# Optimization experiments

Measured on AMD Instinct MI355X. Metric: run time of the kernel, lower is better.

The kernel has to match this reference:

```python
import jax, jax.numpy as jnp
import numpy as np
from jax.ops import segment_sum, segment_max

N, F, H, HEADS, E, OUT = 50000, 256, 64, 4, 800000, 16


def setup_inputs() -> dict:
    key = jax.random.key(0)
    ks = jax.random.split(key, 16)
    s = 0.05
    return {
        "x": jax.random.normal(ks[0], (N, F), jnp.float32),
        "edge_index": jax.random.randint(ks[1], (2, E), 0, N, jnp.int64),
        # GCN layer params
        "W_gcn1": jax.random.normal(ks[2], (F, H), jnp.float32) * s,
        "b_gcn1": jnp.zeros((H,), jnp.float32),
        "W_gcn2": jax.random.normal(ks[3], (H, OUT), jnp.float32) * s,
        "b_gcn2": jnp.zeros((OUT,), jnp.float32),
        # GAT layer 1 (heads=HEADS, concat)
        "W_gat1": jax.random.normal(ks[4], (F, HEADS * H), jnp.float32) * s,
        "a_src1": jax.random.normal(ks[5], (HEADS, H), jnp.float32) * s,
        "a_dst1": jax.random.normal(ks[6], (HEADS, H), jnp.float32) * s,
        "b_gat1": jnp.zeros((HEADS * H,), jnp.float32),
        # GAT layer 2 (heads=1, concat=False)
        "W_gat2": jax.random.normal(ks[7], (HEADS * H, OUT), jnp.float32) * s,
        "a_src2": jax.random.normal(ks[8], (1, OUT), jnp.float32) * s,
        "a_dst2": jax.random.normal(ks[9], (1, OUT), jnp.float32) * s,
        "b_gat2": jnp.zeros((OUT,), jnp.float32),
    }


def _add_self_loops(edge_index, n):
    loop = jnp.arange(n, dtype=edge_index.dtype)
    src = jnp.concatenate([edge_index[0], loop])
    dst = jnp.concatenate([edge_index[1], loop])
    return src, dst


def _gcn(x, src, dst, norm, W, b, n):
    h = x @ W  # [N, out]
    out = segment_sum(h[src] * norm[:, None], dst, num_segments=n)
    return out + b


def _gat(x, src, dst, W, a_s, a_d, b, heads, concat, n):
    h = (x @ W).reshape(n, heads, -1)  # [N, heads, C]
    s_src = jnp.einsum("nhc,hc->nh", h, a_s)
    s_dst = jnp.einsum("nhc,hc->nh", h, a_d)
    e = jax.nn.leaky_relu(s_src[src] + s_dst[dst], 0.2)  # [Etot, heads]
    m = segment_max(e, dst, num_segments=n)               # per-dst softmax
    p = jnp.exp(e - m[dst])
    denom = segment_sum(p, dst, num_segments=n)
    alpha = p / denom[dst]
    out = segment_sum(h[src] * alpha[..., None], dst, num_segments=n)
    out = out.reshape(n, -1) if concat else out.mean(axis=1)
    return out + b


def reference(x, edge_index, W_gcn1, b_gcn1, W_gcn2, b_gcn2,
              W_gat1, a_src1, a_dst1, b_gat1,
              W_gat2, a_src2, a_dst2, b_gat2):
    n = x.shape[0]
    src, dst = _add_self_loops(edge_index, n)
    # symmetric GCN normalization on self-loop-augmented graph
    deg = segment_sum(jnp.ones_like(dst, x.dtype), dst, num_segments=n)
    dinv = jnp.where(deg > 0, jax.lax.rsqrt(deg), 0.0)
    norm = dinv[src] * dinv[dst]

    x_gcn = jax.nn.relu(_gcn(x, src, dst, norm, W_gcn1, b_gcn1, n))
    x_gcn = _gcn(x_gcn, src, dst, norm, W_gcn2, b_gcn2, n)

    x_gat = jax.nn.relu(_gat(x, src, dst, W_gat1, a_src1, a_dst1, b_gat1, HEADS, True, n))
    x_gat = _gat(x_gat, src, dst, W_gat2, a_src2, a_dst2, b_gat2, 1, False, n)

    return jnp.concatenate([x_gcn, x_gat], axis=1)
```

## Files before the change

kernel.cpp:

```cpp
#include <hip/hip_runtime.h>
#include <math.h>

#define NN     50000
#define FF     256
#define HH     64
#define NHEADS 4
#define EE     800000
#define OUTD   16

typedef __attribute__((ext_vector_type(8))) short short8;
typedef __attribute__((ext_vector_type(4))) float f32x4;

__device__ inline unsigned short f2bf(float f) {
    unsigned u = __builtin_bit_cast(unsigned, f);
    unsigned r = (u + 0x7fff + ((u >> 16) & 1)) >> 16;
    return (unsigned short)r;
}
__device__ inline float bf2f(unsigned short s) {
    unsigned u = ((unsigned)s) << 16;
    return __builtin_bit_cast(float, u);
}

__device__ inline void pack_one(const float* __restrict__ W,
                                unsigned short* __restrict__ bhi,
                                unsigned short* __restrict__ blo,
                                int t_, int NT, int NTOT, int TOFF, int SRC_NC) {
    int lane = t_ & 63;
    int tile = (t_ >> 6) % NT;
    int kb = (t_ >> 6) / NT;
    int q = lane >> 4, c = lane & 15;
    size_t off = ((size_t)(kb * NTOT + TOFF + tile) * 64 + lane) * 8;
#pragma unroll
    for (int j = 0; j < 8; j++) {
        float w = W[(size_t)(kb * 32 + q * 8 + j) * SRC_NC + tile * 16 + c];
        unsigned short h = f2bf(w);
        bhi[off + j] = h;
        if (blo) blo[off + j] = f2bf(w - bf2f(h));
    }
}

#define NTT 20
__global__ __launch_bounds__(256) void k_prep(const float* __restrict__ Wg1,
                                              const float* __restrict__ Wgat1,
                                              const float* __restrict__ Wg2,
                                              const float* __restrict__ Wgat2,
                                              unsigned short* __restrict__ bhiC,
                                              unsigned short* __restrict__ bhiG2,
                                              unsigned short* __restrict__ bloG2,
                                              unsigned short* __restrict__ bhiA2,
                                              unsigned short* __restrict__ bloA2,
                                              int* __restrict__ cnt) {
    int t = blockIdx.x * 256 + threadIdx.x;
    if (t < NN) cnt[t] = 0;
    if (t < 2048)        pack_one(Wg1,   bhiC,  nullptr, t,         4,  NTT, 0, 64);
    else if (t < 10240)  pack_one(Wgat1, bhiC,  nullptr, t - 2048,  16, NTT, 4, 256);
    else if (t < 10368)  pack_one(Wg2,   bhiG2, bloG2,   t - 10240, 1,  1,   0, 16);
    else if (t < 10880)  pack_one(Wgat2, bhiA2, bloA2,   t - 10368, 1,  1,   0, 16);
}

__global__ void k_count(const int* __restrict__ dst, int* __restrict__ cnt, int e) {
    int i = blockIdx.x * blockDim.x + threadIdx.x;
    if (i < e) atomicAdd(&cnt[dst[i]], 1);
}

__global__ __launch_bounds__(256) void k_scan_a(const int* __restrict__ cnt,
                                                int* __restrict__ partial, int n) {
    int i = blockIdx.x * 256 + threadIdx.x;
    int v = (i < n) ? cnt[i] : 0;
#pragma unroll
    for (int off = 32; off >= 1; off >>= 1) v += __shfl_xor(v, off, 64);
    __shared__ int ws[4];
    int wave = threadIdx.x >> 6;
    if ((threadIdx.x & 63) == 0) ws[wave] = v;
    __syncthreads();
    if (threadIdx.x == 0) partial[blockIdx.x] = ws[0] + ws[1] + ws[2] + ws[3];
}

__global__ __launch_bounds__(256) void k_scan_b(const int* __restrict__ partial,
                                                int* __restrict__ blockoff,
                                                int* __restrict__ total_out, int nb) {
    __shared__ int arr[256];
    int tid = threadIdx.x;
    arr[tid] = (tid < nb) ? partial[tid] : 0;
    __syncthreads();
#pragma unroll
    for (int off = 1; off < 256; off <<= 1) {
        int v = arr[tid];
        int add = (tid >= off) ? arr[tid - off] : 0;
        __syncthreads();
        arr[tid] = v + add;
        __syncthreads();
    }
    if (tid < nb) blockoff[tid] = arr[tid] - partial[tid];
    if (tid == 0) *total_out = arr[255];
}

__global__ __launch_bounds__(256) void k_scan_c(const int* __restrict__ cnt,
                                                const int* __restrict__ blockoff,
                                                int* __restrict__ row_start,
                                                int* __restrict__ cursor,
                                                float* __restrict__ dinv, int n) {
    __shared__ int arr[256];
    int tid = threadIdx.x;
    int i = blockIdx.x * 256 + tid;
    int c = (i < n) ? cnt[i] : 0;
    arr[tid] = c;
    __syncthreads();
#pragma unroll
    for (int off = 1; off < 256; off <<= 1) {
        int v = arr[tid];
        int add = (tid >= off) ? arr[tid - off] : 0;
        __syncthreads();
        arr[tid] = v + add;
        __syncthreads();
    }
    if (i < n) {
        int excl = arr[tid] - c + blockoff[blockIdx.x];
        row_start[i] = excl;
        cursor[i] = excl;
        dinv[i] = rsqrtf((float)(c + 1));
    }
}

__global__ void k_fill(const int* __restrict__ src, const int* __restrict__ dst,
                       int* __restrict__ cursor, int* __restrict__ col, int e) {
    int i = blockIdx.x * blockDim.x + threadIdx.x;
    if (i < e) {
        int d = dst[i];
        int pos = atomicAdd(&cursor[d], 1);
        col[pos] = src[i];
    }
}

__global__ __launch_bounds__(512, 4) void mfma_gemm_fused(const float* __restrict__ A,
                                                       const unsigned short* __restrict__ Bhi,
                                                       unsigned short* __restrict__ Ch1,
                                                       unsigned char* __restrict__ Chg,
                                                       float* __restrict__ scl,
                                                       const float* __restrict__ dinv,
                                                       const float* __restrict__ a_s,
                                                       const float* __restrict__ a_d,
                                                       float* __restrict__ ssrc,
                                                       float* __restrict__ sdst,
                                                       int M) {
    const int K = 256;
    int tid = threadIdx.x;
    int w = tid >> 6, lane = tid & 63, q = lane >> 4, c = lane & 15;
    int rg = w & 3;
    int half = w >> 2;
    const int T0 = half * 10;
    int row_base = blockIdx.x * 64 + rg * 16;
    int ar = min(row_base + c, M - 1);
    const float* ap = A + (size_t)ar * K + q * 8;

    __shared__ unsigned short ldsB[2][NTT * 512];

    auto stage = [&](int kb, int buf) {
        const char* srcb = (const char*)Bhi + (size_t)kb * (NTT * 1024);
#pragma unroll
        for (int cch = 0; cch < 3; cch++) {
            int ch = w + cch * 8;
            if (ch < NTT) {
                __builtin_amdgcn_global_load_lds(
                    (const unsigned int*)(srcb + ch * 1024 + lane * 16),
                    (unsigned int*)((char*)&ldsB[buf][0] + ch * 1024),
                    16, 0, 0);
            }
        }
    };

    f32x4 acc[10];
#pragma unroll
    for (int t = 0; t < 10; t++) acc[t] = (f32x4){0.f, 0.f, 0.f, 0.f};

    float av[8];
    *(float4*)(av)     = *(const float4*)(ap);
    *(float4*)(av + 4) = *(const float4*)(ap + 4);
    stage(0, 0);
    __syncthreads();

    int buf = 0;
#pragma unroll
    for (int kb = 0; kb < 8; kb++) {
        if (kb < 7) stage(kb + 1, buf ^ 1);
        short8 ahi, alo;
#pragma unroll
        for (int j = 0; j < 8; j++) {
            unsigned short h = f2bf(av[j]);
            ahi[j] = (short)h;
            alo[j] = (short)f2bf(av[j] - bf2f(h));
        }
        if (kb < 7) {
            *(float4*)(av)     = *(const float4*)(ap + (kb + 1) * 32);
            *(float4*)(av + 4) = *(const float4*)(ap + (kb + 1) * 32 + 4);
        }
        const char* bbase = (const char*)&ldsB[buf][0] + lane * 16;
#pragma unroll
        for (int lt = 0; lt < 10; lt++) {
            short8 b = *(const short8*)(bbase + (size_t)(T0 + lt) * 1024);
            acc[lt] = __builtin_amdgcn_mfma_f32_16x16x32_bf16(ahi, b, acc[lt], 0, 0, 0);
            acc[lt] = __builtin_amdgcn_mfma_f32_16x16x32_bf16(alo, b, acc[lt], 0, 0, 0);
        }
        __syncthreads();
        buf ^= 1;
    }

    __shared__ float s_ss[2][64][4];
    __shared__ float s_sd[2][64][4];
    __shared__ float s_mx[2][64];

#pragma unroll
    for (int i = 0; i < 4; i++) {
        int lr = rg * 16 + q * 4 + i;
        float ss[4] = {0.f, 0.f, 0.f, 0.f};
        float sd[4] = {0.f, 0.f, 0.f, 0.f};
        float m = 0.f;
#pragma unroll
        for (int lt = 0; lt < 10; lt++) {
            int gt = T0 + lt;
            if (gt >= 4) {
                int t = gt - 4;
                float v = acc[lt][i];
                ss[t >> 2] += v * a_s[t * 16 + c];
                sd[t >> 2] += v * a_d[t * 16 + c];
                m = fmaxf(m, fabsf(v));
            }
        }
#pragma unroll
        for (int h = 0; h < 4; h++) {
#pragma unroll
            for (int off = 1; off <= 8; off <<= 1) {
                ss[h] += __shfl_xor(ss[h], off, 16);
                sd[h] += __shfl_xor(sd[h], off, 16);
            }
        }
#pragma unroll
        for (int off = 1; off <= 8; off <<= 1) m = fmaxf(m, __shfl_xor(m, off, 16));
        if (c == i) {
#pragma unroll
            for (int h = 0; h < 4; h++) {
                s_ss[half][lr][h] = ss[h];
                s_sd[half][lr][h] = sd[h];
            }
            s_mx[half][lr] = m;
        }
    }
    __syncthreads();

#pragma unroll
    for (int i = 0; i < 4; i++) {
        int lr = rg * 16 + q * 4 + i;
        int r = row_base + q * 4 + i;
        float m = fmaxf(fmaxf(s_mx[0][lr], s_mx[1][lr]), 1e-20f);
        float inv = 127.0f / m;
        if (half == 0 && c == i && r < M) {
            *(float4*)(ssrc + (size_t)r * 4) =
                make_float4(s_ss[0][lr][0] + s_ss[1][lr][0], s_ss[0][lr][1] + s_ss[1][lr][1],
                            s_ss[0][lr][2] + s_ss[1][lr][2], s_ss[0][lr][3] + s_ss[1][lr][3]);
            *(float4*)(sdst + (size_t)r * 4) =
                make_float4(s_sd[0][lr][0] + s_sd[1][lr][0], s_sd[0][lr][1] + s_sd[1][lr][1],
                            s_sd[0][lr][2] + s_sd[1][lr][2], s_sd[0][lr][3] + s_sd[1][lr][3]);
            scl[r] = m * (1.0f / 127.0f);
        }
        if (r < M) {
            if (half == 0) {
                float sc = dinv[r];
#pragma unroll
                for (int lt = 0; lt < 4; lt++)
                    Ch1[(size_t)r * 64 + lt * 16 + c] = f2bf(acc[lt][i] * sc);
            }
#pragma unroll
            for (int lt = 0; lt < 10; lt++) {
                int gt = T0 + lt;
                if (gt >= 4) {
                    int t = gt - 4;
                    int qv = (int)rintf(acc[lt][i] * inv) + 128;
                    Chg[(size_t)r * 256 + t * 16 + c] = (unsigned char)qv;
                }
            }
        }
    }
}

template <int KB, bool SCALE, bool SC2, int OFS>
__device__ inline void n16_body(int bx, int tid,
                                const unsigned short* __restrict__ A,
                                const unsigned short* __restrict__ Bhi,
                                const unsigned short* __restrict__ Blo,
                                unsigned short* __restrict__ Cbf,
                                const float* __restrict__ rowscale,
                                const float* __restrict__ a_s2,
                                const float* __restrict__ a_d2,
                                float* __restrict__ s2s,
                                float* __restrict__ s2d, int M) {
    const int K = KB * 32;
    int w = tid >> 6, lane = tid & 63, q = lane >> 4, c = lane & 15;
    int row_base = bx * 64 + w * 16;
    int ar = min(row_base + c, M - 1);
    const unsigned short* ap = A + (size_t)ar * K + q * 8;
    f32x4 acc = (f32x4){0.f, 0.f, 0.f, 0.f};
#pragma unroll
    for (int kb = 0; kb < KB; kb++) {
        short8 av = *(const short8*)(ap + kb * 32);
        size_t bo = ((size_t)kb * 64 + lane) * 8;
        short8 bh = *(const short8*)(Bhi + bo);
        short8 bl = *(const short8*)(Blo + bo);
        acc = __builtin_amdgcn_mfma_f32_16x16x32_bf16(av, bh, acc, 0, 0, 0);
        acc = __builtin_amdgcn_mfma_f32_16x16x32_bf16(av, bl, acc, 0, 0, 0);
    }
    if (SC2) {
#pragma unroll
        for (int i = 0; i < 4; i++) {
            float ps = acc[i] * a_s2[c];
            float pd = acc[i] * a_d2[c];
#pragma unroll
            for (int off = 1; off <= 8; off <<= 1) {
                ps += __shfl_xor(ps, off, 16);
                pd += __shfl_xor(pd, off, 16);
            }
            int r = row_base + q * 4 + i;
            if (c == i && r < M) {
                s2s[r] = ps;
                s2d[r] = pd;
            }
        }
    }
#pragma unroll
    for (int i = 0; i < 4; i++) {
        int r = row_base + q * 4 + i;
        if (r < M) {
            float sc = SCALE ? rowscale[r] : 1.0f;
            Cbf[((size_t)r * 16 + c) * 2 + OFS] = f2bf(acc[i] * sc);
        }
    }
}

__global__ __launch_bounds__(256) void mfma_n16_both(const unsigned short* __restrict__ Ag,
                                                     const unsigned short* __restrict__ Ac,
                                                     const unsigned short* __restrict__ bhiA2,
                                                     const unsigned short* __restrict__ bloA2,
                                                     const unsigned short* __restrict__ bhiG2,
                                                     const unsigned short* __restrict__ bloG2,
                                                     unsigned short* __restrict__ pairb,
                                                     const float* __restrict__ dinv,
                                                     const float* __restrict__ a_s2,
                                                     const float* __restrict__ a_d2,
                                                     float* __restrict__ s2s,
                                                     float* __restrict__ s2d,
                                                     int M, int GB) {
    int bx = blockIdx.x;
    if (bx < GB)
        n16_body<8, false, true, 1>(bx, threadIdx.x, Ag, bhiA2, bloA2, pairb,
                                    nullptr, a_s2, a_d2, s2s, s2d, M);
    else
        n16_body<2, true, false, 0>(bx - GB, threadIdx.x, Ac, bhiG2, bloG2, pairb,
                                    dinv, nullptr, nullptr, nullptr, nullptr, M);
}

__global__ __launch_bounds__(256) void both_agg(const unsigned char* __restrict__ hg,
                                                const unsigned short* __restrict__ h1,
                                                const float* __restrict__ scl,
                                                const int* __restrict__ rs,
                                                const int* __restrict__ col,
                                                const float* __restrict__ ssrc,
                                                const float* __restrict__ sdst,
                                                const float* __restrict__ dinv,
                                                const float* __restrict__ bgat,
                                                const float* __restrict__ bgcn,
                                                unsigned short* __restrict__ outg,
                                                unsigned short* __restrict__ outc) {
    __shared__ int s_lds[4][64];
    __shared__ float p_lds[4][64 * 4];
    int tid = threadIdx.x;
    int w = tid >> 6, lane = tid & 63;
    int wid = blockIdx.x * 4 + w;
    int hh = lane >> 4;
    int cidx = (lane & 15) * 4;
    int* sl = s_lds[w];
    float* pl = p_lds[w];

    float di = dinv[wid];
    float4 sd4 = *(const float4*)(sdst + (size_t)wid * 4);
    float sdv[4] = {sd4.x, sd4.y, sd4.z, sd4.w};
    float4 sf4 = *(const float4*)(ssrc + (size_t)wid * 4);
    float sfv[4] = {sf4.x, sf4.y, sf4.z, sf4.w};
    float psf[4];
#pragma unroll
    for (int h = 0; h < 4; h++) {
        float e = sfv[h] + sdv[h];
        e = (e >= 0.f) ? e : 0.2f * e;
        psf[h] = __expf(e);
    }
    float pse = (hh & 2) ? ((hh & 1) ? psf[3] : psf[2]) : ((hh & 1) ? psf[1] : psf[0]);
    float pses = pse * scl[wid];
    const unsigned char* hbase = hg + lane * 4;
    unsigned hv0 = *(const unsigned*)(hbase + (size_t)wid * 256);
    float4 acc;
    acc.x = ((float)(hv0 & 0xffu) - 128.f) * pses;
    acc.y = ((float)((hv0 >> 8) & 0xffu) - 128.f) * pses;
    acc.z = ((float)((hv0 >> 16) & 0xffu) - 128.f) * pses;
    acc.w = ((float)(hv0 >> 24) - 128.f) * pses;
    float accb = 0.f;
    float4 accc = make_float4(0.f, 0.f, 0.f, 0.f);

    float lsum[4] = {0.f, 0.f, 0.f, 0.f};
    int beg = rs[wid], end = rs[wid + 1];
    for (int j0 = beg; j0 < end; j0 += 64) {
        int cnt = min(64, end - j0);
        if (lane < cnt) {
            int sreg = col[j0 + lane];
            float ssc = scl[sreg];
            float4 sv = *(const float4*)(ssrc + (size_t)sreg * 4);
            float svv[4] = {sv.x, sv.y, sv.z, sv.w};
            float pv[4];
#pragma unroll
            for (int h = 0; h < 4; h++) {
                float e = svv[h] + sdv[h];
                e = (e >= 0.f) ? e : 0.2f * e;
                pv[h] = __expf(e);
                lsum[h] += pv[h];
            }
            sl[lane] = sreg;
            *(float4*)&pl[lane * 4] =
                make_float4(pv[0] * ssc, pv[1] * ssc, pv[2] * ssc, pv[3] * ssc);
        }
        int e = 0;
        for (; e + 4 <= cnt; e += 4) {
            int s0 = sl[e], s1 = sl[e + 1], s2 = sl[e + 2], s3 = sl[e + 3];
            float p0 = pl[e * 4 + hh], p1 = pl[(e + 1) * 4 + hh];
            float p2 = pl[(e + 2) * 4 + hh], p3 = pl[(e + 3) * 4 + hh];
            unsigned v0 = *(const unsigned*)(hbase + (size_t)s0 * 256);
            unsigned v1 = *(const unsigned*)(hbase + (size_t)s1 * 256);
            unsigned v2 = *(const unsigned*)(hbase + (size_t)s2 * 256);
            unsigned v3 = *(const unsigned*)(hbase + (size_t)s3 * 256);
            acc.x += (float)(v0 & 0xffu) * p0;
            acc.y += (float)((v0 >> 8) & 0xffu) * p0;
            acc.z += (float)((v0 >> 16) & 0xffu) * p0;
            acc.w += (float)(v0 >> 24) * p0;
            acc.x += (float)(v1 & 0xffu) * p1;
            acc.y += (float)((v1 >> 8) & 0xffu) * p1;
            acc.z += (float)((v1 >> 16) & 0xffu) * p1;
            acc.w += (float)(v1 >> 24) * p1;
            acc.x += (float)(v2 & 0xffu) * p2;
            acc.y += (float)((v2 >> 8) & 0xffu) * p2;
            acc.z += (float)((v2 >> 16) & 0xffu) * p2;
            acc.w += (float)(v2 >> 24) * p2;
            acc.x += (float)(v3 & 0xffu) * p3;
            acc.y += (float)((v3 >> 8) & 0xffu) * p3;
            acc.z += (float)((v3 >> 16) & 0xffu) * p3;
            acc.w += (float)(v3 >> 24) * p3;
            accb += (p0 + p1) + (p2 + p3);
        }
        for (; e < cnt; e++) {
            int s = sl[e];
            float p = pl[e * 4 + hh];
            unsigned v = *(const unsigned*)(hbase + (size_t)s * 256);
            acc.x += (float)(v & 0xffu) * p;
            acc.y += (float)((v >> 8) & 0xffu) * p;
            acc.z += (float)((v >> 16) & 0xffu) * p;
            acc.w += (float)(v >> 24) * p;
            accb += p;
        }
        int e2 = hh;
        for (; e2 + 4 < cnt; e2 += 8) {
            int sa = sl[e2], sb = sl[e2 + 4];
            ushort4 va = *(const ushort4*)(h1 + (size_t)sa * HH + cidx);
            ushort4 vb = *(const ushort4*)(h1 + (size_t)sb * HH + cidx);
            accc.x += bf2f(va.x) + bf2f(vb.x);
            accc.y += bf2f(va.y) + bf2f(vb.y);
            accc.z += bf2f(va.z) + bf2f(vb.z);
            accc.w += bf2f(va.w) + bf2f(vb.w);
        }
        if (e2 < cnt) {
            int sa = sl[e2];
            ushort4 va = *(const ushort4*)(h1 + (size_t)sa * HH + cidx);
            accc.x += bf2f(va.x); accc.y += bf2f(va.y);
            accc.z += bf2f(va.z); accc.w += bf2f(va.w);
        }
    }
    float corr = 128.0f * accb;
    acc.x -= corr; acc.y -= corr; acc.z -= corr; acc.w -= corr;
#pragma unroll
    for (int h = 0; h < 4; h++) {
        float v = lsum[h];
        for (int off = 32; off >= 1; off >>= 1) v += __shfl_xor(v, off, 64);
        lsum[h] = v + psf[h];
    }
    float lt = (hh & 2) ? ((hh & 1) ? lsum[3] : lsum[2]) : ((hh & 1) ? lsum[1] : lsum[0]);
    float li = 1.0f / lt;
    float4 bv = *(const float4*)(bgat + lane * 4);
    ushort4 o;
    o.x = f2bf(fmaxf(acc.x * li + bv.x, 0.f));
    o.y = f2bf(fmaxf(acc.y * li + bv.y, 0.f));
    o.z = f2bf(fmaxf(acc.z * li + bv.z, 0.f));
    o.w = f2bf(fmaxf(acc.w * li + bv.w, 0.f));
    *(ushort4*)(outg + (size_t)wid * 256 + lane * 4) = o;
#pragma unroll
    for (int off = 16; off <= 32; off <<= 1) {
        accc.x += __shfl_xor(accc.x, off, 64);
        accc.y += __shfl_xor(accc.y, off, 64);
        accc.z += __shfl_xor(accc.z, off, 64);
        accc.w += __shfl_xor(accc.w, off, 64);
    }
    if (hh == 0) {
        ushort4 sv = *(const ushort4*)(h1 + (size_t)wid * HH + cidx);
        float4 bc = *(const float4*)(bgcn + cidx);
        ushort4 oc;
        oc.x = f2bf(fmaxf((accc.x + bf2f(sv.x)) * di + bc.x, 0.f));
        oc.y = f2bf(fmaxf((accc.y + bf2f(sv.y)) * di + bc.y, 0.f));
        oc.z = f2bf(fmaxf((accc.z + bf2f(sv.z)) * di + bc.z, 0.f));
        oc.w = f2bf(fmaxf((accc.w + bf2f(sv.w)) * di + bc.w, 0.f));
        *(ushort4*)(outc + (size_t)wid * HH + cidx) = oc;
    }
}

__global__ __launch_bounds__(256) void final_agg(const unsigned* __restrict__ hp,
                                                 const int* __restrict__ rs,
                                                 const int* __restrict__ col,
                                                 const float* __restrict__ dinv,
                                                 const float* __restrict__ s2s,
                                                 const float* __restrict__ s2d,
                                                 const float* __restrict__ bg2,
                                                 const float* __restrict__ bga2,
                                                 float* __restrict__ out) {
    int t = blockIdx.x * 256 + threadIdx.x;
    int node = t >> 4;
    int c = t & 15;
    float di = dinv[node];
    float sd = s2d[node];
    float es = s2s[node] + sd;
    es = (es >= 0.f) ? es : 0.2f * es;
    float psf = __expf(es);
    unsigned pvs = hp[(size_t)node * 16 + c];
    float accg = bf2f((unsigned short)pvs);
    float acca = bf2f((unsigned short)(pvs >> 16)) * psf;
    float lp = 0.f;
    int beg = rs[node], end = rs[node + 1];
    for (int j0 = beg; j0 < end; j0 += 16) {
        int cnt = min(16, end - j0);
        int sreg = 0;
        float pr = 0.f;
        if (c < cnt) {
            sreg = col[j0 + c];
            float e = s2s[sreg] + sd;
            e = (e >= 0.f) ? e : 0.2f * e;
            pr = __expf(e);
            lp += pr;
        }
        for (int e = 0; e < cnt; e += 4) {
            int si[4];
            float pi[4];
#pragma unroll
            for (int u = 0; u < 4; u++) {
                si[u] = __shfl(sreg, (e + u) & 15, 16);
                pi[u] = __shfl(pr, (e + u) & 15, 16);
            }
            unsigned hv[4];
#pragma unroll
            for (int u = 0; u < 4; u++) hv[u] = hp[(size_t)si[u] * 16 + c];
#pragma unroll
            for (int u = 0; u < 4; u++) {
                if (e + u < cnt) {
                    accg += bf2f((unsigned short)hv[u]);
                    acca += bf2f((unsigned short)(hv[u] >> 16)) * pi[u];
                }
            }
        }
    }
    for (int off = 8; off >= 1; off >>= 1) lp += __shfl_xor(lp, off, 16);
    float l = lp + psf;
    out[(size_t)node * 32 + c] = accg * di + bg2[c];
    out[(size_t)node * 32 + 16 + c] = acca / l + bga2[c];
}

extern "C" void kernel_launch(void* const* d_in, const int* in_sizes, int n_in,
                              void* d_out, int out_size, void* d_ws, size_t ws_size,
                              hipStream_t stream) {
    const float* x      = (const float*)d_in[0];
    const int*   ei     = (const int*)d_in[1];
    const float* Wg1    = (const float*)d_in[2];
    const float* bg1    = (const float*)d_in[3];
    const float* Wg2    = (const float*)d_in[4];
    const float* bg2    = (const float*)d_in[5];
    const float* Wgat1  = (const float*)d_in[6];
    const float* a_src1 = (const float*)d_in[7];
    const float* a_dst1 = (const float*)d_in[8];
    const float* bgat1  = (const float*)d_in[9];
    const float* Wgat2  = (const float*)d_in[10];
    const float* a_src2 = (const float*)d_in[11];
    const float* a_dst2 = (const float*)d_in[12];
    const float* bgat2  = (const float*)d_in[13];
    float* out = (float*)d_out;

    const int* e_src = ei;
    const int* e_dst = ei + EE;

    char* wsb = (char*)d_ws;
    size_t o = 0;
    auto alloc = [&](size_t bytes) -> void* {
        void* p = wsb + o;
        o += (bytes + 255) & ~(size_t)255;
        return p;
    };
    float* dinv            = (float*)alloc(NN * 4);
    float* ssrc1           = (float*)alloc((size_t)NN * 16);
    float* sdst1           = (float*)alloc((size_t)NN * 16);
    unsigned short* h1b    = (unsigned short*)alloc((size_t)NN * HH * 2);
    unsigned short* xg1    = (unsigned short*)alloc((size_t)NN * HH * 2);
    unsigned char*  hgb    = (unsigned char*)alloc((size_t)NN * 256);
    float* sclb            = (float*)alloc(NN * 4);
    unsigned short* xgat1  = (unsigned short*)alloc((size_t)NN * 256 * 2);
    unsigned short* pairb  = (unsigned short*)alloc((size_t)NN * 16 * 4);
    float* s2src           = (float*)alloc(NN * 4);
    float* s2dst           = (float*)alloc(NN * 4);
    unsigned short* bhiC   = (unsigned short*)alloc((size_t)8 * NTT * 512 * 2);
    unsigned short* bhiG2  = (unsigned short*)alloc(64 * 16 * 2);
    unsigned short* bloG2  = (unsigned short*)alloc(64 * 16 * 2);
    unsigned short* bhiA2  = (unsigned short*)alloc(256 * 16 * 2);
    unsigned short* bloA2  = (unsigned short*)alloc(256 * 16 * 2);
    int* cnt               = (int*)alloc(NN * 4);
    int* rowstart          = (int*)alloc((NN + 1) * 4);
    int* cursor            = (int*)alloc(NN * 4);
    int* colarr            = (int*)alloc((size_t)EE * 4);
    int* partial           = (int*)alloc(256 * 4);
    int* blockoff          = (int*)alloc(256 * 4);

    const int TB = 256;
    const int NB = (NN + 255) / 256;
    k_prep<<<NB, TB, 0, stream>>>(Wg1, Wgat1, Wg2, Wgat2,
                                  bhiC, bhiG2, bloG2, bhiA2, bloA2, cnt);
    k_count<<<(EE + TB - 1) / TB, TB, 0, stream>>>(e_dst, cnt, EE);
    k_scan_a<<<NB, TB, 0, stream>>>(cnt, partial, NN);
    k_scan_b<<<1, TB, 0, stream>>>(partial, blockoff, rowstart + NN, NB);
    k_scan_c<<<NB, TB, 0, stream>>>(cnt, blockoff, rowstart, cursor, dinv, NN);
    k_fill<<<(EE + TB - 1) / TB, TB, 0, stream>>>(e_src, e_dst, cursor, colarr, EE);

    const int GB = (NN + 63) / 64;
    const int G16 = (NN * 16) / 256;

    mfma_gemm_fused<<<GB, 512, 0, stream>>>(x, bhiC, h1b, hgb, sclb, dinv,
                                            a_src1, a_dst1, ssrc1, sdst1, NN);

    both_agg<<<NN / 4, TB, 0, stream>>>(hgb, h1b, sclb, rowstart, colarr, ssrc1, sdst1,
                                        dinv, bgat1, bg1, xgat1, xg1);

    mfma_n16_both<<<2 * GB, TB, 0, stream>>>(xgat1, xg1, bhiA2, bloA2, bhiG2, bloG2,
                                             pairb, dinv, a_src2, a_dst2,
                                             s2src, s2dst, NN, GB);

    final_agg<<<G16, TB, 0, stream>>>((const unsigned*)pairb, rowstart, colarr, dinv,
                                      s2src, s2dst, bg2, bgat2, out);
}
```

Before: 327.1 us.

## Fuse second-layer projections into aggregation kernel epilogue with LDS weights

Removes the separate layer-2 MFMA GEMM kernel and instead computes the 256x16 GAT and 64x16 GCN projections per node inside both_agg, using fp32 weights staged in shared memory. This drops the bf16 round trip of the intermediate xgat1/xg1 activations through global memory, one kernel launch and the hi/lo weight packing. In exchange, every block reloads about 20KB of weights into LDS, raising LDS use per block and possibly lowering occupancy, and the per-wave scalar FMA loop replaces MFMA work.

Measured after the change: 368.4 us. +12.6%, slower.

```diff
diff --git a/kernel.cpp b/kernel.cpp
--- a/kernel.cpp
+++ b/kernel.cpp
@@ -23,7 +23,6 @@
 
 __device__ inline void pack_one(const float* __restrict__ W,
                                 unsigned short* __restrict__ bhi,
-                                unsigned short* __restrict__ blo,
                                 int t_, int NT, int NTOT, int TOFF, int SRC_NC) {
     int lane = t_ & 63;
     int tile = (t_ >> 6) % NT;
@@ -33,29 +32,19 @@
 #pragma unroll
     for (int j = 0; j < 8; j++) {
         float w = W[(size_t)(kb * 32 + q * 8 + j) * SRC_NC + tile * 16 + c];
-        unsigned short h = f2bf(w);
-        bhi[off + j] = h;
-        if (blo) blo[off + j] = f2bf(w - bf2f(h));
+        bhi[off + j] = f2bf(w);
     }
 }
 
 #define NTT 20
 __global__ __launch_bounds__(256) void k_prep(const float* __restrict__ Wg1,
                                               const float* __restrict__ Wgat1,
-                                              const float* __restrict__ Wg2,
-                                              const float* __restrict__ Wgat2,
                                               unsigned short* __restrict__ bhiC,
-                                              unsigned short* __restrict__ bhiG2,
-                                              unsigned short* __restrict__ bloG2,
-                                              unsigned short* __restrict__ bhiA2,
-                                              unsigned short* __restrict__ bloA2,
                                               int* __restrict__ cnt) {
     int t = blockIdx.x * 256 + threadIdx.x;
     if (t < NN) cnt[t] = 0;
-    if (t < 2048)        pack_one(Wg1,   bhiC,  nullptr, t,         4,  NTT, 0, 64);
-    else if (t < 10240)  pack_one(Wgat1, bhiC,  nullptr, t - 2048,  16, NTT, 4, 256);
-    else if (t < 10368)  pack_one(Wg2,   bhiG2, bloG2,   t - 10240, 1,  1,   0, 16);
-    else if (t < 10880)  pack_one(Wgat2, bhiA2, bloA2,   t - 10368, 1,  1,   0, 16);
+    if (t < 2048)        pack_one(Wg1,   bhiC, t,         4,  NTT, 0, 64);
+    else if (t < 10240)  pack_one(Wgat1, bhiC, t - 2048,  16, NTT, 4, 256);
 }
 
 __global__ void k_count(const int* __restrict__ dst, int* __restrict__ cnt, int e) {
@@ -282,81 +271,6 @@
     }
 }
 
-template <int KB, bool SCALE, bool SC2, int OFS>
-__device__ inline void n16_body(int bx, int tid,
-                                const unsigned short* __restrict__ A,
-                                const unsigned short* __restrict__ Bhi,
-                                const unsigned short* __restrict__ Blo,
-                                unsigned short* __restrict__ Cbf,
-                                const float* __restrict__ rowscale,
-                                const float* __restrict__ a_s2,
-                                const float* __restrict__ a_d2,
-                                float* __restrict__ s2s,
-                                float* __restrict__ s2d, int M) {
-    const int K = KB * 32;
-    int w = tid >> 6, lane = tid & 63, q = lane >> 4, c = lane & 15;
-    int row_base = bx * 64 + w * 16;
-    int ar = min(row_base + c, M - 1);
-    const unsigned short* ap = A + (size_t)ar * K + q * 8;
-    f32x4 acc = (f32x4){0.f, 0.f, 0.f, 0.f};
-#pragma unroll
-    for (int kb = 0; kb < KB; kb++) {
-        short8 av = *(const short8*)(ap + kb * 32);
-        size_t bo = ((size_t)kb * 64 + lane) * 8;
-        short8 bh = *(const short8*)(Bhi + bo);
-        short8 bl = *(const short8*)(Blo + bo);
-        acc = __builtin_amdgcn_mfma_f32_16x16x32_bf16(av, bh, acc, 0, 0, 0);
-        acc = __builtin_amdgcn_mfma_f32_16x16x32_bf16(av, bl, acc, 0, 0, 0);
-    }
-    if (SC2) {
-#pragma unroll
-        for (int i = 0; i < 4; i++) {
-            float ps = acc[i] * a_s2[c];
-            float pd = acc[i] * a_d2[c];
-#pragma unroll
-            for (int off = 1; off <= 8; off <<= 1) {
-                ps += __shfl_xor(ps, off, 16);
-                pd += __shfl_xor(pd, off, 16);
-            }
-            int r = row_base + q * 4 + i;
-            if (c == i && r < M) {
-                s2s[r] = ps;
-                s2d[r] = pd;
-            }
-        }
-    }
-#pragma unroll
-    for (int i = 0; i < 4; i++) {
-        int r = row_base + q * 4 + i;
-        if (r < M) {
-            float sc = SCALE ? rowscale[r] : 1.0f;
-            Cbf[((size_t)r * 16 + c) * 2 + OFS] = f2bf(acc[i] * sc);
-        }
-    }
-}
-
-__global__ __launch_bounds__(256) void mfma_n16_both(const unsigned short* __restrict__ Ag,
-                                                     const unsigned short* __restrict__ Ac,
-                                                     const unsigned short* __restrict__ bhiA2,
-                                                     const unsigned short* __restrict__ bloA2,
-                                                     const unsigned short* __restrict__ bhiG2,
-                                                     const unsigned short* __restrict__ bloG2,
-                                                     unsigned short* __restrict__ pairb,
-                                                     const float* __restrict__ dinv,
-                                                     const float* __restrict__ a_s2,
-                                                     const float* __restrict__ a_d2,
-                                                     float* __restrict__ s2s,
-                                                     float* __restrict__ s2d,
-                                                     int M, int GB) {
-    int bx = blockIdx.x;
-    if (bx < GB)
-        n16_body<8, false, true, 1>(bx, threadIdx.x, Ag, bhiA2, bloA2, pairb,
-                                    nullptr, a_s2, a_d2, s2s, s2d, M);
-    else
-        n16_body<2, true, false, 0>(bx - GB, threadIdx.x, Ac, bhiG2, bloG2, pairb,
-                                    dinv, nullptr, nullptr, nullptr, nullptr, M);
-}
-
 __global__ __launch_bounds__(256) void both_agg(const unsigned char* __restrict__ hg,
                                                 const unsigned short* __restrict__ h1,
                                                 const float* __restrict__ scl,
@@ -367,10 +281,17 @@
                                                 const float* __restrict__ dinv,
                                                 const float* __restrict__ bgat,
                                                 const float* __restrict__ bgcn,
-                                                unsigned short* __restrict__ outg,
-                                                unsigned short* __restrict__ outc) {
+                                                const float* __restrict__ Wg2f,
+                                                const float* __restrict__ Wga2f,
+                                                const float* __restrict__ a_s2,
+                                                const float* __restrict__ a_d2,
+                                                unsigned* __restrict__ pairb,
+                                                float* __restrict__ s2s,
+                                                float* __restrict__ s2d) {
     __shared__ int s_lds[4][64];
-    __shared__ float p_lds[4][64 * 4];
+    __shared__ float p_lds[4][256];
+    __shared__ float w2a[256 * 16];
+    __shared__ float w2g[64 * 16];
     int tid = threadIdx.x;
     int w = tid >> 6, lane = tid & 63;
     int wid = blockIdx.x * 4 + w;
@@ -378,6 +299,10 @@
     int cidx = (lane & 15) * 4;
     int* sl = s_lds[w];
     float* pl = p_lds[w];
+
+    for (int idx = tid; idx < 256 * 16; idx += 256) w2a[idx] = Wga2f[idx];
+    for (int idx = tid; idx < 64 * 16; idx += 256) w2g[idx] = Wg2f[idx];
+    __syncthreads();
 
     float di = dinv[wid];
     float4 sd4 = *(const float4*)(sdst + (size_t)wid * 4);
@@ -489,12 +414,11 @@
     float lt = (hh & 2) ? ((hh & 1) ? lsum[3] : lsum[2]) : ((hh & 1) ? lsum[1] : lsum[0]);
     float li = 1.0f / lt;
     float4 bv = *(const float4*)(bgat + lane * 4);
-    ushort4 o;
-    o.x = f2bf(fmaxf(acc.x * li + bv.x, 0.f));
-    o.y = f2bf(fmaxf(acc.y * li + bv.y, 0.f));
-    o.z = f2bf(fmaxf(acc.z * li + bv.z, 0.f));
-    o.w = f2bf(fmaxf(acc.w * li + bv.w, 0.f));
-    *(ushort4*)(outg + (size_t)wid * 256 + lane * 4) = o;
+    float ox = fmaxf(acc.x * li + bv.x, 0.f);
+    float oy = fmaxf(acc.y * li + bv.y, 0.f);
+    float oz = fmaxf(acc.z * li + bv.z, 0.f);
+    float ow = fmaxf(acc.w * li + bv.w, 0.f);
+    *(float4*)&pl[lane * 4] = make_float4(ox, oy, oz, ow);
 #pragma unroll
     for (int off = 16; off <= 32; off <<= 1) {
         accc.x += __shfl_xor(accc.x, off, 64);
@@ -502,15 +426,49 @@
         accc.z += __shfl_xor(accc.z, off, 64);
         accc.w += __shfl_xor(accc.w, off, 64);
     }
+    float* slf = (float*)sl;
     if (hh == 0) {
         ushort4 sv = *(const ushort4*)(h1 + (size_t)wid * HH + cidx);
         float4 bc = *(const float4*)(bgcn + cidx);
-        ushort4 oc;
-        oc.x = f2bf(fmaxf((accc.x + bf2f(sv.x)) * di + bc.x, 0.f));
-        oc.y = f2bf(fmaxf((accc.y + bf2f(sv.y)) * di + bc.y, 0.f));
-        oc.z = f2bf(fmaxf((accc.z + bf2f(sv.z)) * di + bc.z, 0.f));
-        oc.w = f2bf(fmaxf((accc.w + bf2f(sv.w)) * di + bc.w, 0.f));
-        *(ushort4*)(outc + (size_t)wid * HH + cidx) = oc;
+        slf[cidx + 0] = fmaxf((accc.x + bf2f(sv.x)) * di + bc.x, 0.f);
+        slf[cidx + 1] = fmaxf((accc.y + bf2f(sv.y)) * di + bc.y, 0.f);
+        slf[cidx + 2] = fmaxf((accc.z + bf2f(sv.z)) * di + bc.z, 0.f);
+        slf[cidx + 3] = fmaxf((accc.w + bf2f(sv.w)) * di + bc.w, 0.f);
+    }
+    int j = lane & 15, g = lane >> 4;
+    float a2 = 0.f;
+#pragma unroll
+    for (int i0 = 0; i0 < 64; i0 += 4) {
+        float4 xv = *(float4*)&pl[g * 64 + i0];
+        int ch = g * 64 + i0;
+        a2 += xv.x * w2a[(ch + 0) * 16 + j];
+        a2 += xv.y * w2a[(ch + 1) * 16 + j];
+        a2 += xv.z * w2a[(ch + 2) * 16 + j];
+        a2 += xv.w * w2a[(ch + 3) * 16 + j];
+    }
+    float g2 = 0.f;
+#pragma unroll
+    for (int i0 = 0; i0 < 16; i0 += 4) {
+        float4 xv = *(float4*)&slf[g * 16 + i0];
+        int ch = g * 16 + i0;
+        g2 += xv.x * w2g[(ch + 0) * 16 + j];
+        g2 += xv.y * w2g[(ch + 1) * 16 + j];
+        g2 += xv.z * w2g[(ch + 2) * 16 + j];
+        g2 += xv.w * w2g[(ch + 3) * 16 + j];
+    }
+    a2 += __shfl_xor(a2, 16, 64); a2 += __shfl_xor(a2, 32, 64);
+    g2 += __shfl_xor(g2, 16, 64); g2 += __shfl_xor(g2, 32, 64);
+    float ps = a2 * a_s2[j];
+    float pd = a2 * a_d2[j];
+#pragma unroll
+    for (int off = 1; off <= 8; off <<= 1) {
+        ps += __shfl_xor(ps, off, 16);
+        pd += __shfl_xor(pd, off, 16);
+    }
+    if (lane == 0) { s2s[wid] = ps; s2d[wid] = pd; }
+    if (lane < 16) {
+        unsigned pack = ((unsigned)f2bf(a2) << 16) | (unsigned)f2bf(g2 * di);
+        pairb[(size_t)wid * 16 + j] = pack;
     }
 }
 
@@ -606,18 +564,12 @@
     float* ssrc1           = (float*)alloc((size_t)NN * 16);
     float* sdst1           = (float*)alloc((size_t)NN * 16);
     unsigned short* h1b    = (unsigned short*)alloc((size_t)NN * HH * 2);
-    unsigned short* xg1    = (unsigned short*)alloc((size_t)NN * HH * 2);
     unsigned char*  hgb    = (unsigned char*)alloc((size_t)NN * 256);
     float* sclb            = (float*)alloc(NN * 4);
-    unsigned short* xgat1  = (unsigned short*)alloc((size_t)NN * 256 * 2);
-    unsigned short* pairb  = (unsigned short*)alloc((size_t)NN * 16 * 4);
+    unsigned* pairb        = (unsigned*)alloc((size_t)NN * 16 * 4);
     float* s2src           = (float*)alloc(NN * 4);
     float* s2dst           = (float*)alloc(NN * 4);
     unsigned short* bhiC   = (unsigned short*)alloc((size_t)8 * NTT * 512 * 2);
-    unsigned short* bhiG2  = (unsigned short*)alloc(64 * 16 * 2);
-    unsigned short* bloG2  = (unsigned short*)alloc(64 * 16 * 2);
-    unsigned short* bhiA2  = (unsigned short*)alloc(256 * 16 * 2);
-    unsigned short* bloA2  = (unsigned short*)alloc(256 * 16 * 2);
     int* cnt               = (int*)alloc(NN * 4);
     int* rowstart          = (int*)alloc((NN + 1) * 4);
     int* cursor            = (int*)alloc(NN * 4);
@@ -627,8 +579,7 @@
 
     const int TB = 256;
     const int NB = (NN + 255) / 256;
-    k_prep<<<NB, TB, 0, stream>>>(Wg1, Wgat1, Wg2, Wgat2,
-                                  bhiC, bhiG2, bloG2, bhiA2, bloA2, cnt);
+    k_prep<<<NB, TB, 0, stream>>>(Wg1, Wgat1, bhiC, cnt);
     k_count<<<(EE + TB - 1) / TB, TB, 0, stream>>>(e_dst, cnt, EE);
     k_scan_a<<<NB, TB, 0, stream>>>(cnt, partial, NN);
     k_scan_b<<<1, TB, 0, stream>>>(partial, blockoff, rowstart + NN, NB);
@@ -641,13 +592,11 @@
     mfma_gemm_fused<<<GB, 512, 0, stream>>>(x, bhiC, h1b, hgb, sclb, dinv,
                                             a_src1, a_dst1, ssrc1, sdst1, NN);
 
-    both_agg<<<NN / 4, TB, 0, stream>>>(hgb, h1b, sclb, rowstart, colarr, ssrc1, sdst1,
-                                        dinv, bgat1, bg1, xgat1, xg1);
-
-    mfma_n16_both<<<2 * GB, TB, 0, stream>>>(xgat1, xg1, bhiA2, bloA2, bhiG2, bloG2,
-                                             pairb, dinv, a_src2, a_dst2,
-                                             s2src, s2dst, NN, GB);
-
-    final_agg<<<G16, TB, 0, stream>>>((const unsigned*)pairb, rowstart, colarr, dinv,
+    both_agg<<<NN / 4, TB, 0, stream>>>(hgb, h1b, sclb, rowstart, colarr,
+                                        ssrc1, sdst1, dinv, bgat1, bg1,
+                                        Wg2, Wgat2, a_src2, a_dst2,
+                                        pairb, s2src, s2dst);
+
+    final_agg<<<G16, TB, 0, stream>>>(pairb, rowstart, colarr, dinv,
                                       s2src, s2dst, bg2, bgat2, out);
 }
```

## Fuse edge counting into GEMM launch and defer dinv scaling to fill kernel

Applied to the files above, without the earlier changes.

Runs the destination-degree count as extra blocks inside the first GEMM launch, so the atomic counting no longer needs its own kernel and can run concurrently with the GEMM. The GEMM no longer depends on dinv and writes unscaled bf16 h1. A new fill_scale kernel combines the CSR fill with an elementwise pass that multiplies h1 by dinv in place. This removes two launches and lets independent work overlap, at the cost of an extra read-modify-write pass over h1 and a second bf16 rounding of it.

Result: faster. 311.6 us, median of 2 (-4.8%).

```diff
diff --git a/kernel.cpp b/kernel.cpp
--- a/kernel.cpp
+++ b/kernel.cpp
@@ -58,11 +58,6 @@
     else if (t < 10880)  pack_one(Wgat2, bhiA2, bloA2,   t - 10368, 1,  1,   0, 16);
 }
 
-__global__ void k_count(const int* __restrict__ dst, int* __restrict__ cnt, int e) {
-    int i = blockIdx.x * blockDim.x + threadIdx.x;
-    if (i < e) atomicAdd(&cnt[dst[i]], 1);
-}
-
 __global__ __launch_bounds__(256) void k_scan_a(const int* __restrict__ cnt,
                                                 int* __restrict__ partial, int n) {
     int i = blockIdx.x * 256 + threadIdx.x;
@@ -122,27 +117,52 @@
     }
 }
 
-__global__ void k_fill(const int* __restrict__ src, const int* __restrict__ dst,
-                       int* __restrict__ cursor, int* __restrict__ col, int e) {
-    int i = blockIdx.x * blockDim.x + threadIdx.x;
-    if (i < e) {
-        int d = dst[i];
-        int pos = atomicAdd(&cursor[d], 1);
-        col[pos] = src[i];
-    }
-}
-
-__global__ __launch_bounds__(512, 4) void mfma_gemm_fused(const float* __restrict__ A,
-                                                       const unsigned short* __restrict__ Bhi,
-                                                       unsigned short* __restrict__ Ch1,
-                                                       unsigned char* __restrict__ Chg,
-                                                       float* __restrict__ scl,
-                                                       const float* __restrict__ dinv,
-                                                       const float* __restrict__ a_s,
-                                                       const float* __restrict__ a_d,
-                                                       float* __restrict__ ssrc,
-                                                       float* __restrict__ sdst,
-                                                       int M) {
+__global__ __launch_bounds__(256) void fill_scale(const int* __restrict__ src,
+                                                  const int* __restrict__ dst,
+                                                  int* __restrict__ cursor,
+                                                  int* __restrict__ col,
+                                                  unsigned short* __restrict__ h1,
+                                                  const float* __restrict__ dinv,
+                                                  int FB) {
+    int bx = blockIdx.x;
+    if (bx < FB) {
+        int i = bx * 256 + threadIdx.x;
+        if (i < EE) {
+            int d = dst[i];
+            int pos = atomicAdd(&cursor[d], 1);
+            col[pos] = src[i];
+        }
+    } else {
+        int t = (bx - FB) * 256 + threadIdx.x;
+        if (t < NN * HH / 8) {
+            int r = t >> 3;
+            float sc = dinv[r];
+            short8 v = *(short8*)(h1 + (size_t)t * 8);
+#pragma unroll
+            for (int j = 0; j < 8; j++)
+                v[j] = (short)f2bf(bf2f((unsigned short)v[j]) * sc);
+            *(short8*)(h1 + (size_t)t * 8) = v;
+        }
+    }
+}
+
+__global__ __launch_bounds__(512, 4) void gemm_count(const float* __restrict__ A,
+                                                     const unsigned short* __restrict__ Bhi,
+                                                     unsigned short* __restrict__ Ch1,
+                                                     unsigned char* __restrict__ Chg,
+                                                     float* __restrict__ scl,
+                                                     const float* __restrict__ a_s,
+                                                     const float* __restrict__ a_d,
+                                                     float* __restrict__ ssrc,
+                                                     float* __restrict__ sdst,
+                                                     const int* __restrict__ e_dst,
+                                                     int* __restrict__ cnt,
+                                                     int M, int GBp) {
+    if (blockIdx.x >= GBp) {
+        int i = (blockIdx.x - GBp) * 512 + threadIdx.x;
+        if (i < EE) atomicAdd(&cnt[e_dst[i]], 1);
+        return;
+    }
     const int K = 256;
     int tid = threadIdx.x;
     int w = tid >> 6, lane = tid & 63, q = lane >> 4, c = lane & 15;
@@ -264,10 +284,9 @@
         }
         if (r < M) {
             if (half == 0) {
-                float sc = dinv[r];
 #pragma unroll
                 for (int lt = 0; lt < 4; lt++)
-                    Ch1[(size_t)r * 64 + lt * 16 + c] = f2bf(acc[lt][i] * sc);
+                    Ch1[(size_t)r * 64 + lt * 16 + c] = f2bf(acc[lt][i]);
             }
 #pragma unroll
             for (int lt = 0; lt < 10; lt++) {
@@ -627,19 +646,22 @@
 
     const int TB = 256;
     const int NB = (NN + 255) / 256;
+    const int GB = (NN + 63) / 64;
+    const int CB = (EE + 511) / 512;
+    const int FB = (EE + 255) / 256;
+    const int SB = (NN * HH / 8 + 255) / 256;
+    const int G16 = (NN * 16) / 256;
+
     k_prep<<<NB, TB, 0, stream>>>(Wg1, Wgat1, Wg2, Wgat2,
                                   bhiC, bhiG2, bloG2, bhiA2, bloA2, cnt);
-    k_count<<<(EE + TB - 1) / TB, TB, 0, stream>>>(e_dst, cnt, EE);
+    gemm_count<<<GB + CB, 512, 0, stream>>>(x, bhiC, h1b, hgb, sclb,
+                                            a_src1, a_dst1, ssrc1, sdst1,
+                                            e_dst, cnt, NN, GB);
     k_scan_a<<<NB, TB, 0, stream>>>(cnt, partial, NN);
     k_scan_b<<<1, TB, 0, stream>>>(partial, blockoff, rowstart + NN, NB);
     k_scan_c<<<NB, TB, 0, stream>>>(cnt, blockoff, rowstart, cursor, dinv, NN);
-    k_fill<<<(EE + TB - 1) / TB, TB, 0, stream>>>(e_src, e_dst, cursor, colarr, EE);
-
-    const int GB = (NN + 63) / 64;
-    const int G16 = (NN * 16) / 256;
-
-    mfma_gemm_fused<<<GB, 512, 0, stream>>>(x, bhiC, h1b, hgb, sclb, dinv,
-                                            a_src1, a_dst1, ssrc1, sdst1, NN);
+    fill_scale<<<FB + SB, TB, 0, stream>>>(e_src, e_dst, cursor, colarr,
+                                           h1b, dinv, FB);
 
     both_agg<<<NN / 4, TB, 0, stream>>>(hgb, h1b, sclb, rowstart, colarr, ssrc1, sdst1,
                                         dinv, bgat1, bg1, xgat1, xg1);
```
